# Optimization experiments

Hardware: AMD Instinct MI355X
Metric: run time of the kernel (lower is better)

The kernel has to match this reference:

```python
import jax, jax.numpy as jnp
import numpy as np

B, T, H, W, C = 2, 6, 16, 16, 256
NUM_HEADS = 8


def light_cone_mask(T, H, W):
    """Boolean mask [N, N] (N = T*H*W): key (t,h,w) is visible to query
    (tq,hq,wq) iff t <= tq and |h-hq|, |w-wq| <= radius(tq, t), where
    radius = int(1 + (max(H,W)-1) * (tq-t) / max(tq,1))  (per the torch loop)."""
    M = max(H, W)
    tq = jnp.arange(T)[:, None]
    tk = jnp.arange(T)[None, :]
    # values are >= 0 on the causal region, so floor == int() truncation
    r = jnp.floor(1.0 + (M - 1) * (tq - tk) / jnp.maximum(tq, 1)).astype(jnp.int32)  # [T,T]
    causal = tk <= tq  # [T,T]
    dh = jnp.abs(jnp.arange(H)[:, None] - jnp.arange(H)[None, :])  # [Hq,Hk]
    dw = jnp.abs(jnp.arange(W)[:, None] - jnp.arange(W)[None, :])  # [Wq,Wk]
    m = (causal[:, None, None, :, None, None]
         & (dh[None, :, None, None, :, None] <= r[:, None, None, :, None, None])
         & (dw[None, None, :, None, None, :] <= r[:, None, None, :, None, None]))
    return m.reshape(T * H * W, T * H * W)


def setup_inputs() -> dict:
    key = jax.random.key(0)
    k1, k2, k3 = jax.random.split(key, 3)
    x = jax.random.normal(k1, (B, T, H, W, C), dtype=jnp.float32)
    Wqkv = jax.random.normal(k2, (C, 3 * C), dtype=jnp.float32) * 0.02
    Wo = jax.random.normal(k3, (C, C), dtype=jnp.float32) * 0.02
    bo = jnp.zeros((C,), dtype=jnp.float32)
    return {"x": x, "Wqkv": Wqkv, "Wo": Wo, "bo": bo}


def reference(x, Wqkv, Wo, bo):
    Bx, Tx, Hx, Wx, Cx = x.shape
    nh = NUM_HEADS
    hd = Cx // nh
    scale = hd ** (-0.5)
    N = Tx * Hx * Wx
    xt = x.reshape(Bx, N, Cx)
    qkv = (xt @ Wqkv).reshape(Bx, N, 3, nh, hd)
    q = qkv[:, :, 0].transpose(0, 2, 1, 3)  # [B, nh, N, hd]
    k = qkv[:, :, 1].transpose(0, 2, 1, 3)
    v = qkv[:, :, 2].transpose(0, 2, 1, 3)
    scores = jnp.einsum("bhqd,bhkd->bhqk", q, k) * scale  # [B, nh, N, N]
    mask = light_cone_mask(Tx, Hx, Wx)  # [N, N]
    neg = jnp.asarray(-1e9, dtype=scores.dtype)
    scores = jnp.where(mask[None, None, :, :], scores, neg)
    attn = jax.nn.softmax(scores, axis=-1)
    out = jnp.einsum("bhqk,bhkd->bhqd", attn, v)  # [B, nh, N, hd]
    out = out.transpose(0, 2, 1, 3).reshape(Bx, N, Cx)
    out = out @ Wo + bo
    return out.reshape(Bx, Tx, Hx, Wx, Cx)
```

## Files before the change

kernel.cpp:

```cpp
#include <hip/hip_runtime.h>
#include <hip/hip_bf16.h>

#define BB   2
#define TT   6
#define HH   16
#define WW   16
#define CC   256
#define NH   8
#define HD   32
#define NN   (TT*HH*WW)
#define BN   (BB*NN)
#define SCALE 0.17677669529663687f

typedef __attribute__((ext_vector_type(8))) short bf16x8;
typedef __attribute__((ext_vector_type(4))) short bf16x4;
typedef __attribute__((ext_vector_type(4))) float f32x4;
typedef __attribute__((ext_vector_type(16))) float f32x16;

static __device__ inline short f2b(float x) {
    __hip_bfloat16 h = __float2bfloat16(x);
    return __builtin_bit_cast(short, h);
}

__global__ __launch_bounds__(256) void gemm1_qkv(const float* __restrict__ x,
                                                 const float* __restrict__ Wqkv,
                                                 short* __restrict__ Qb,
                                                 short* __restrict__ Kb,
                                                 short* __restrict__ VT) {
    const int w = threadIdx.x >> 6, lane = threadIdx.x & 63;
    const int g = lane >> 4, c16 = lane & 15;
    const int W = blockIdx.x * 4 + w;
    const int ct = W % 12;
    const int n0 = ct * 64;
    const int mw = (W / 12) * 32;
    f32x4 acc[2][4] = {};
    #pragma unroll
    for (int ks = 0; ks < 8; ++ks) {
        const int k0 = ks * 32;
        const float* ap0 = x + (size_t)(mw + c16) * 256 + k0 + 8 * g;
        const float* ap1 = ap0 + 16 * 256;
        const float4 fa = *(const float4*)ap0;
        const float4 fb = *(const float4*)(ap0 + 4);
        const float4 fc = *(const float4*)ap1;
        const float4 fd = *(const float4*)(ap1 + 4);
        short ta[8] = { f2b(fa.x), f2b(fa.y), f2b(fa.z), f2b(fa.w),
                        f2b(fb.x), f2b(fb.y), f2b(fb.z), f2b(fb.w) };
        short tb[8] = { f2b(fc.x), f2b(fc.y), f2b(fc.z), f2b(fc.w),
                        f2b(fd.x), f2b(fd.y), f2b(fd.z), f2b(fd.w) };
        const bf16x8 a0 = *(bf16x8*)ta;
        const bf16x8 a1 = *(bf16x8*)tb;
        #pragma unroll
        for (int ni = 0; ni < 4; ++ni) {
            const float* wp = Wqkv + (size_t)(k0 + 8 * g) * 768 + n0 + ni * 16 + c16;
            short tw[8];
            #pragma unroll
            for (int i = 0; i < 8; ++i) tw[i] = f2b(wp[(size_t)i * 768]);
            const bf16x8 bfr = *(bf16x8*)tw;
            acc[0][ni] = __builtin_amdgcn_mfma_f32_16x16x32_bf16(a0, bfr, acc[0][ni], 0, 0, 0);
            acc[1][ni] = __builtin_amdgcn_mfma_f32_16x16x32_bf16(a1, bfr, acc[1][ni], 0, 0, 0);
        }
    }
    const int sec = ct >> 2;
    #pragma unroll
    for (int mi = 0; mi < 2; ++mi) {
        const int brow = mw + mi * 16;
        const int b = brow >= NN;
        const int nbase = brow - b * NN;
        #pragma unroll
        for (int ni = 0; ni < 4; ++ni) {
            const int col = n0 + ni * 16;
            const int h  = (col >> 5) & 7;
            const int d0 = col & 31;
            const int bh = b * 8 + h;
            if (sec == 2) {
                short t4[4];
                #pragma unroll
                for (int r = 0; r < 4; ++r) t4[r] = f2b(acc[mi][ni][r]);
                const int kt  = nbase >> 5;
                const int klo = (nbase & 16) + 4 * g;
                size_t off = ((size_t)((bh * 48 + kt) * 32) + d0 + c16) * 32 + klo;
                *(bf16x4*)(VT + off) = *(bf16x4*)t4;
            } else {
                short* dst = (sec == 0) ? Qb : Kb;
                const float sc = (sec == 0) ? SCALE : 1.f;
                #pragma unroll
                for (int r = 0; r < 4; ++r)
                    dst[((size_t)bh * NN + nbase + 4 * g + r) * 32 + d0 + c16] =
                        f2b(acc[mi][ni][r] * sc);
            }
        }
    }
}

__global__ __launch_bounds__(256) void attn_mfma32(const short* __restrict__ Qb,
                                                   const short* __restrict__ Kb,
                                                   const short* __restrict__ VT,
                                                   short* __restrict__ aob) {
    const int w    = threadIdx.x >> 6;
    const int lane = threadIdx.x & 63;
    const int l31  = lane & 31;
    const int gb   = lane >> 5;
    const int wq   = lane & 15;
    const int qh   = (lane >> 4) & 1;
    const int task = blockIdx.x;
    const int qt = task % 48, bh = task / 48;
    const int tqp = qt >> 4, hq = qt & 15;
    const int tq_a = 2 * tqp, tq_b = tq_a + 1;

    __shared__ int desc[64];
    __shared__ float sm_l[4][64];
    __shared__ float sm_acc[4][64][17];

    const int tq_l = qh ? tq_b : tq_a;
    const int qn   = tq_l * 256 + hq * 16 + wq;
    const short* QBH = Qb + (size_t)bh * NN * 32;
    const bf16x8 qf0 = *(const bf16x8*)(QBH + (size_t)qn * 32 + 8 * gb);
    const bf16x8 qf1 = *(const bf16x8*)(QBH + (size_t)qn * 32 + 16 + 8 * gb);

    int dwv[8];
    #pragma unroll
    for (int i = 0; i < 8; ++i) {
        int kl = (i & 3) + 8 * (i >> 2) + 4 * gb;
        int d = kl - wq; dwv[i] = d < 0 ? -d : d;
    }

    const int tqm_a = tq_a ? tq_a : 1;
    int ntiles = 0;
    int cst[6], h20[6], rtav[6], rtbv[6];
    #pragma unroll
    for (int tk = 0; tk < 6; ++tk) {
        int rb = 1 + (15 * (tq_b - tk)) / tq_b;
        int ra = (tk <= tq_a) ? (1 + (15 * (tq_a - tk)) / tqm_a) : -1;
        int lo = hq - rb; lo = lo < 0 ? 0 : lo;
        int hi = hq + rb; hi = hi > 15 ? 15 : hi;
        int c  = (tk <= tq_b) ? ((hi >> 1) - (lo >> 1) + 1) : 0;
        cst[tk] = ntiles; h20[tk] = lo >> 1; rtav[tk] = ra; rtbv[tk] = rb;
        ntiles += c;
    }

    if (w == 0) {
        const int t = lane;
        int dsc = 255;
        if (t < ntiles) {
            int sel = 0;
            #pragma unroll
            for (int tk = 1; tk < 6; ++tk)
                if (tk <= tq_b && t >= cst[tk]) sel = tk;
            const int hk2 = h20[sel] + (t - cst[sel]);
            dsc = ((sel * 256 + hk2 * 32) << 16) | ((rtav[sel] & 255) << 8) | (rtbv[sel] & 255);
        }
        desc[t] = dsc;
    }
    __syncthreads();

    const short* KBH = Kb + (size_t)bh * NN * 32;
    const short* VBH = VT + (size_t)bh * 48 * 32 * 32;

    f32x16 acc, zf16;
    #pragma unroll
    for (int r = 0; r < 16; ++r) { acc[r] = 0.f; zf16[r] = 0.f; }
    float l_run = 0.f;

    int pi = w;
    int dc = 0;
    bf16x8 kf0c = {}, kf1c = {}, vf0c = {}, vf1c = {};
    if (pi < ntiles) {
        dc = desc[pi];
        const int kb = dc >> 16;
        kf0c = *(const bf16x8*)(KBH + (size_t)(kb + l31) * 32 + 8 * gb);
        kf1c = *(const bf16x8*)(KBH + (size_t)(kb + l31) * 32 + 16 + 8 * gb);
        vf0c = *(const bf16x8*)(VBH + (size_t)((kb >> 5) * 32 + l31) * 32 + 8 * gb);
        vf1c = *(const bf16x8*)(VBH + (size_t)((kb >> 5) * 32 + l31) * 32 + 16 + 8 * gb);
    }
    while (pi < ntiles) {
        const int pn = pi + 4;
        const int pc = pn < ntiles ? pn : pi;
        const int dn = desc[pc];
        const int kbn = dn >> 16;
        const bf16x8 kf0n = *(const bf16x8*)(KBH + (size_t)(kbn + l31) * 32 + 8 * gb);
        const bf16x8 kf1n = *(const bf16x8*)(KBH + (size_t)(kbn + l31) * 32 + 16 + 8 * gb);
        const bf16x8 vf0n = *(const bf16x8*)(VBH + (size_t)((kbn >> 5) * 32 + l31) * 32 + 8 * gb);
        const bf16x8 vf1n = *(const bf16x8*)(VBH + (size_t)((kbn >> 5) * 32 + l31) * 32 + 16 + 8 * gb);

        const int rta = (dc << 16) >> 24;
        const int rtb = (dc << 24) >> 24;
        const int rt_l = qh ? rtb : rta;
        const int hk2 = (dc >> 21) & 7;
        const int t0 = 2 * hk2 - hq;
        const int dh0 = t0 < 0 ? -t0 : t0;
        const int t1 = t0 + 1;
        const int dh1 = t1 < 0 ? -t1 : t1;
        const bool A0 = dh0 <= rt_l, A1 = dh1 <= rt_l;
        bool dok[8];
        #pragma unroll
        for (int i = 0; i < 8; ++i) dok[i] = dwv[i] <= rt_l;

        f32x16 s = __builtin_amdgcn_mfma_f32_32x32x16_bf16(kf0c, qf0, zf16, 0, 0, 0);
        s = __builtin_amdgcn_mfma_f32_32x32x16_bf16(kf1c, qf1, s, 0, 0, 0);

        float p[16];
        #pragma unroll
        for (int r = 0; r < 16; ++r) {
            const bool ok = (r < 8 ? A0 : A1) && dok[r & 7];
            p[r] = ok ? __expf(s[r]) : 0.f;
        }
        float ps = (((p[0] + p[1]) + (p[2] + p[3])) + ((p[4] + p[5]) + (p[6] + p[7])))
                 + (((p[8] + p[9]) + (p[10] + p[11])) + ((p[12] + p[13]) + (p[14] + p[15])));
        l_run += ps;

        unsigned u[8];
        #pragma unroll
        for (int j = 0; j < 8; ++j)
            asm("v_cvt_pk_bf16_f32 %0, %1, %2" : "=v"(u[j]) : "v"(p[2 * j]), "v"(p[2 * j + 1]));
        asm volatile("v_permlane32_swap_b32 %0, %1" : "+v"(u[0]), "+v"(u[2]));
        asm volatile("v_permlane32_swap_b32 %0, %1" : "+v"(u[1]), "+v"(u[3]));
        asm volatile("v_permlane32_swap_b32 %0, %1" : "+v"(u[4]), "+v"(u[6]));
        asm volatile("v_permlane32_swap_b32 %0, %1" : "+v"(u[5]), "+v"(u[7]));
        const int4 b1i = { (int)u[0], (int)u[1], (int)u[2], (int)u[3] };
        const int4 b2i = { (int)u[4], (int)u[5], (int)u[6], (int)u[7] };
        const bf16x8 pb1 = __builtin_bit_cast(bf16x8, b1i);
        const bf16x8 pb2 = __builtin_bit_cast(bf16x8, b2i);

        acc = __builtin_amdgcn_mfma_f32_32x32x16_bf16(vf0c, pb1, acc, 0, 0, 0);
        acc = __builtin_amdgcn_mfma_f32_32x32x16_bf16(vf1c, pb2, acc, 0, 0, 0);

        pi = pn; dc = dn;
        kf0c = kf0n; kf1c = kf1n; vf0c = vf0n; vf1c = vf1n;
    }

    sm_l[w][lane] = l_run;
    #pragma unroll
    for (int r = 0; r < 16; ++r) sm_acc[w][lane][r] = acc[r];
    __syncthreads();
    if (w == 0) {
        const float lt = (sm_l[0][l31] + sm_l[0][l31 + 32])
                       + (sm_l[1][l31] + sm_l[1][l31 + 32])
                       + (sm_l[2][l31] + sm_l[2][l31 + 32])
                       + (sm_l[3][l31] + sm_l[3][l31 + 32]);
        const float inv = 1.f / lt;
        short* op = aob + ((size_t)(bh >> 3) * NN + qn) * CC + (bh & 7) * 32;
        #pragma unroll
        for (int j = 0; j < 4; ++j) {
            short t4[4];
            #pragma unroll
            for (int s2 = 0; s2 < 4; ++s2) {
                const int r = 4 * j + s2;
                const float a = sm_acc[0][lane][r] + sm_acc[1][lane][r]
                              + sm_acc[2][lane][r] + sm_acc[3][lane][r];
                t4[s2] = f2b(a * inv);
            }
            *(bf16x4*)(op + 8 * j + 4 * gb) = *(bf16x4*)t4;
        }
    }
}

__global__ __launch_bounds__(256) void gemm2_out(const short* __restrict__ aob,
                                                 const float* __restrict__ Wo,
                                                 const float* __restrict__ bias,
                                                 float* __restrict__ out) {
    const int w = threadIdx.x >> 6, lane = threadIdx.x & 63;
    const int g = lane >> 4, c16 = lane & 15;
    const int W = blockIdx.x * 4 + w;
    const int n0 = (W & 3) * 64;
    const int mw = (W >> 2) * 32;
    f32x4 acc[2][4] = {};
    #pragma unroll
    for (int ks = 0; ks < 8; ++ks) {
        const int k0 = ks * 32;
        const bf16x8 a0 = *(const bf16x8*)(aob + (size_t)(mw + c16) * 256 + k0 + g * 8);
        const bf16x8 a1 = *(const bf16x8*)(aob + (size_t)(mw + 16 + c16) * 256 + k0 + g * 8);
        #pragma unroll
        for (int ni = 0; ni < 4; ++ni) {
            const float* wp = Wo + (size_t)(k0 + 8 * g) * 256 + n0 + ni * 16 + c16;
            short tw[8];
            #pragma unroll
            for (int i = 0; i < 8; ++i) tw[i] = f2b(wp[(size_t)i * 256]);
            const bf16x8 bfr = *(bf16x8*)tw;
            acc[0][ni] = __builtin_amdgcn_mfma_f32_16x16x32_bf16(a0, bfr, acc[0][ni], 0, 0, 0);
            acc[1][ni] = __builtin_amdgcn_mfma_f32_16x16x32_bf16(a1, bfr, acc[1][ni], 0, 0, 0);
        }
    }
    #pragma unroll
    for (int mi = 0; mi < 2; ++mi) {
        #pragma unroll
        for (int ni = 0; ni < 4; ++ni) {
            const int col = n0 + ni * 16 + c16;
            const float bv = bias[col];
            #pragma unroll
            for (int r = 0; r < 4; ++r)
                out[(size_t)(mw + mi * 16 + 4 * g + r) * 256 + col] = acc[mi][ni][r] + bv;
        }
    }
}

extern "C" void kernel_launch(void* const* d_in, const int* in_sizes, int n_in,
                              void* d_out, int out_size, void* d_ws, size_t ws_size,
                              hipStream_t stream) {
    const float* x    = (const float*)d_in[0];
    const float* Wqkv = (const float*)d_in[1];
    const float* Wo   = (const float*)d_in[2];
    const float* bo   = (const float*)d_in[3];
    float* out = (float*)d_out;

    short* Qb  = (short*)d_ws;
    short* Kb  = Qb + 786432;
    short* VT  = Kb + 786432;
    short* aob = VT + 786432;

    gemm1_qkv<<<288, 256, 0, stream>>>(x, Wqkv, Qb, Kb, VT);
    attn_mfma32<<<768, 256, 0, stream>>>(Qb, Kb, VT, aob);
    gemm2_out<<<96, 256, 0, stream>>>(aob, Wo, bo, out);
}
```

Before: 38.87 us.

## Shrink GEMM wave tiles, pre-transpose Wo in attention, spread epilogue over warps

Both projection GEMMs now give each wave a 16-row tile instead of 32 rows, so the grids double from 288 to 576 and from 96 to 192 blocks. In gemm1, waves in a block now share one weight column tile. The first 32 attention blocks convert Wo to a transposed bf16 buffer, which lets gemm2 load vectorised bf16 B fragments instead of eight strided fp32 loads plus conversions. The attention epilogue now splits the cross-wave reduction and store across all four waves instead of only wave 0. The risk is that each wave reloads the same weight fragment for half the work, and a few attention blocks take on the extra Wo conversion.

```diff
diff --git a/kernel.cpp b/kernel.cpp
--- a/kernel.cpp
+++ b/kernel.cpp
@@ -29,26 +29,20 @@
                                                  short* __restrict__ VT) {
     const int w = threadIdx.x >> 6, lane = threadIdx.x & 63;
     const int g = lane >> 4, c16 = lane & 15;
-    const int W = blockIdx.x * 4 + w;
-    const int ct = W % 12;
+    const int ct = blockIdx.x % 12;
+    const int rg = blockIdx.x / 12;
     const int n0 = ct * 64;
-    const int mw = (W / 12) * 32;
-    f32x4 acc[2][4] = {};
+    const int mw = rg * 64 + w * 16;
+    f32x4 acc[4] = {};
     #pragma unroll
     for (int ks = 0; ks < 8; ++ks) {
         const int k0 = ks * 32;
-        const float* ap0 = x + (size_t)(mw + c16) * 256 + k0 + 8 * g;
-        const float* ap1 = ap0 + 16 * 256;
-        const float4 fa = *(const float4*)ap0;
-        const float4 fb = *(const float4*)(ap0 + 4);
-        const float4 fc = *(const float4*)ap1;
-        const float4 fd = *(const float4*)(ap1 + 4);
+        const float* ap = x + (size_t)(mw + c16) * 256 + k0 + 8 * g;
+        const float4 fa = *(const float4*)ap;
+        const float4 fb = *(const float4*)(ap + 4);
         short ta[8] = { f2b(fa.x), f2b(fa.y), f2b(fa.z), f2b(fa.w),
                         f2b(fb.x), f2b(fb.y), f2b(fb.z), f2b(fb.w) };
-        short tb[8] = { f2b(fc.x), f2b(fc.y), f2b(fc.z), f2b(fc.w),
-                        f2b(fd.x), f2b(fd.y), f2b(fd.z), f2b(fd.w) };
         const bf16x8 a0 = *(bf16x8*)ta;
-        const bf16x8 a1 = *(bf16x8*)tb;
         #pragma unroll
         for (int ni = 0; ni < 4; ++ni) {
             const float* wp = Wqkv + (size_t)(k0 + 8 * g) * 768 + n0 + ni * 16 + c16;
@@ -56,38 +50,33 @@
             #pragma unroll
             for (int i = 0; i < 8; ++i) tw[i] = f2b(wp[(size_t)i * 768]);
             const bf16x8 bfr = *(bf16x8*)tw;
-            acc[0][ni] = __builtin_amdgcn_mfma_f32_16x16x32_bf16(a0, bfr, acc[0][ni], 0, 0, 0);
-            acc[1][ni] = __builtin_amdgcn_mfma_f32_16x16x32_bf16(a1, bfr, acc[1][ni], 0, 0, 0);
+            acc[ni] = __builtin_amdgcn_mfma_f32_16x16x32_bf16(a0, bfr, acc[ni], 0, 0, 0);
         }
     }
     const int sec = ct >> 2;
-    #pragma unroll
-    for (int mi = 0; mi < 2; ++mi) {
-        const int brow = mw + mi * 16;
-        const int b = brow >= NN;
-        const int nbase = brow - b * NN;
-        #pragma unroll
-        for (int ni = 0; ni < 4; ++ni) {
-            const int col = n0 + ni * 16;
-            const int h  = (col >> 5) & 7;
-            const int d0 = col & 31;
-            const int bh = b * 8 + h;
-            if (sec == 2) {
-                short t4[4];
-                #pragma unroll
-                for (int r = 0; r < 4; ++r) t4[r] = f2b(acc[mi][ni][r]);
-                const int kt  = nbase >> 5;
-                const int klo = (nbase & 16) + 4 * g;
-                size_t off = ((size_t)((bh * 48 + kt) * 32) + d0 + c16) * 32 + klo;
-                *(bf16x4*)(VT + off) = *(bf16x4*)t4;
-            } else {
-                short* dst = (sec == 0) ? Qb : Kb;
-                const float sc = (sec == 0) ? SCALE : 1.f;
-                #pragma unroll
-                for (int r = 0; r < 4; ++r)
-                    dst[((size_t)bh * NN + nbase + 4 * g + r) * 32 + d0 + c16] =
-                        f2b(acc[mi][ni][r] * sc);
-            }
+    const int b = mw >= NN;
+    const int nbase = mw - b * NN;
+    #pragma unroll
+    for (int ni = 0; ni < 4; ++ni) {
+        const int col = n0 + ni * 16;
+        const int h  = (col >> 5) & 7;
+        const int d0 = col & 31;
+        const int bh = b * 8 + h;
+        if (sec == 2) {
+            short t4[4];
+            #pragma unroll
+            for (int r = 0; r < 4; ++r) t4[r] = f2b(acc[ni][r]);
+            const int kt  = nbase >> 5;
+            const int klo = (nbase & 16) + 4 * g;
+            size_t off = ((size_t)((bh * 48 + kt) * 32) + d0 + c16) * 32 + klo;
+            *(bf16x4*)(VT + off) = *(bf16x4*)t4;
+        } else {
+            short* dst = (sec == 0) ? Qb : Kb;
+            const float sc = (sec == 0) ? SCALE : 1.f;
+            #pragma unroll
+            for (int r = 0; r < 4; ++r)
+                dst[((size_t)bh * NN + nbase + 4 * g + r) * 32 + d0 + c16] =
+                    f2b(acc[ni][r] * sc);
         }
     }
 }
@@ -95,6 +84,8 @@
 __global__ __launch_bounds__(256) void attn_mfma32(const short* __restrict__ Qb,
                                                    const short* __restrict__ Kb,
                                                    const short* __restrict__ VT,
+                                                   const float* __restrict__ Wo,
+                                                   short* __restrict__ woT,
                                                    short* __restrict__ aob) {
     const int w    = threadIdx.x >> 6;
     const int lane = threadIdx.x & 63;
@@ -107,6 +98,16 @@
     const int tqp = qt >> 4, hq = qt & 15;
     const int tq_a = 2 * tqp, tq_b = tq_a + 1;
 
+    if (blockIdx.x < 32) {
+        const int idx = blockIdx.x * 256 + threadIdx.x;
+        const int k0 = (idx & 31) * 8;
+        const int n  = idx >> 5;
+        short t[8];
+        #pragma unroll
+        for (int j = 0; j < 8; ++j) t[j] = f2b(Wo[(size_t)(k0 + j) * 256 + n]);
+        *(bf16x8*)(woT + (size_t)n * 256 + k0) = *(bf16x8*)t;
+    }
+
     __shared__ int desc[64];
     __shared__ float sm_l[4][64];
     __shared__ float sm_acc[4][64][17];
@@ -232,64 +233,51 @@
     #pragma unroll
     for (int r = 0; r < 16; ++r) sm_acc[w][lane][r] = acc[r];
     __syncthreads();
-    if (w == 0) {
+    {
         const float lt = (sm_l[0][l31] + sm_l[0][l31 + 32])
                        + (sm_l[1][l31] + sm_l[1][l31 + 32])
                        + (sm_l[2][l31] + sm_l[2][l31 + 32])
                        + (sm_l[3][l31] + sm_l[3][l31 + 32]);
         const float inv = 1.f / lt;
         short* op = aob + ((size_t)(bh >> 3) * NN + qn) * CC + (bh & 7) * 32;
-        #pragma unroll
-        for (int j = 0; j < 4; ++j) {
-            short t4[4];
-            #pragma unroll
-            for (int s2 = 0; s2 < 4; ++s2) {
-                const int r = 4 * j + s2;
-                const float a = sm_acc[0][lane][r] + sm_acc[1][lane][r]
-                              + sm_acc[2][lane][r] + sm_acc[3][lane][r];
-                t4[s2] = f2b(a * inv);
-            }
-            *(bf16x4*)(op + 8 * j + 4 * gb) = *(bf16x4*)t4;
-        }
+        short t4[4];
+        #pragma unroll
+        for (int s2 = 0; s2 < 4; ++s2) {
+            const int r = 4 * w + s2;
+            const float a = sm_acc[0][lane][r] + sm_acc[1][lane][r]
+                          + sm_acc[2][lane][r] + sm_acc[3][lane][r];
+            t4[s2] = f2b(a * inv);
+        }
+        *(bf16x4*)(op + 8 * w + 4 * gb) = *(bf16x4*)t4;
     }
 }
 
 __global__ __launch_bounds__(256) void gemm2_out(const short* __restrict__ aob,
-                                                 const float* __restrict__ Wo,
+                                                 const short* __restrict__ woT,
                                                  const float* __restrict__ bias,
                                                  float* __restrict__ out) {
     const int w = threadIdx.x >> 6, lane = threadIdx.x & 63;
     const int g = lane >> 4, c16 = lane & 15;
-    const int W = blockIdx.x * 4 + w;
-    const int n0 = (W & 3) * 64;
-    const int mw = (W >> 2) * 32;
-    f32x4 acc[2][4] = {};
+    const int n0 = (blockIdx.x & 3) * 64;
+    const int mw = (blockIdx.x >> 2) * 64 + w * 16;
+    f32x4 acc[4] = {};
     #pragma unroll
     for (int ks = 0; ks < 8; ++ks) {
         const int k0 = ks * 32;
         const bf16x8 a0 = *(const bf16x8*)(aob + (size_t)(mw + c16) * 256 + k0 + g * 8);
-        const bf16x8 a1 = *(const bf16x8*)(aob + (size_t)(mw + 16 + c16) * 256 + k0 + g * 8);
         #pragma unroll
         for (int ni = 0; ni < 4; ++ni) {
-            const float* wp = Wo + (size_t)(k0 + 8 * g) * 256 + n0 + ni * 16 + c16;
-            short tw[8];
-            #pragma unroll
-            for (int i = 0; i < 8; ++i) tw[i] = f2b(wp[(size_t)i * 256]);
-            const bf16x8 bfr = *(bf16x8*)tw;
-            acc[0][ni] = __builtin_amdgcn_mfma_f32_16x16x32_bf16(a0, bfr, acc[0][ni], 0, 0, 0);
-            acc[1][ni] = __builtin_amdgcn_mfma_f32_16x16x32_bf16(a1, bfr, acc[1][ni], 0, 0, 0);
-        }
-    }
-    #pragma unroll
-    for (int mi = 0; mi < 2; ++mi) {
-        #pragma unroll
-        for (int ni = 0; ni < 4; ++ni) {
-            const int col = n0 + ni * 16 + c16;
-            const float bv = bias[col];
-            #pragma unroll
-            for (int r = 0; r < 4; ++r)
-                out[(size_t)(mw + mi * 16 + 4 * g + r) * 256 + col] = acc[mi][ni][r] + bv;
-        }
+            const bf16x8 bfr = *(const bf16x8*)(woT + (size_t)(n0 + ni * 16 + c16) * 256 + k0 + g * 8);
+            acc[ni] = __builtin_amdgcn_mfma_f32_16x16x32_bf16(a0, bfr, acc[ni], 0, 0, 0);
+        }
+    }
+    #pragma unroll
+    for (int ni = 0; ni < 4; ++ni) {
+        const int col = n0 + ni * 16 + c16;
+        const float bv = bias[col];
+        #pragma unroll
+        for (int r = 0; r < 4; ++r)
+            out[(size_t)(mw + 4 * g + r) * 256 + col] = acc[ni][r] + bv;
     }
 }
 
@@ -303,11 +291,12 @@
     float* out = (float*)d_out;
 
     short* Qb  = (short*)d_ws;
-    short* Kb  = Qb + 786432;
-    short* VT  = Kb + 786432;
-    short* aob = VT + 786432;
-
-    gemm1_qkv<<<288, 256, 0, stream>>>(x, Wqkv, Qb, Kb, VT);
-    attn_mfma32<<<768, 256, 0, stream>>>(Qb, Kb, VT, aob);
-    gemm2_out<<<96, 256, 0, stream>>>(aob, Wo, bo, out);
-}
+    short* Kb  = Qb  + 786432;
+    short* VT  = Kb  + 786432;
+    short* aob = VT  + 786432;
+    short* woT = aob + 786432;
+
+    gemm1_qkv<<<576, 256, 0, stream>>>(x, Wqkv, Qb, Kb, VT);
+    attn_mfma32<<<768, 256, 0, stream>>>(Qb, Kb, VT, Wo, woT, aob);
+    gemm2_out<<<192, 256, 0, stream>>>(aob, woT, bo, out);
+}
```

After: 36.67 us. -5.6%, faster.
